# Kernel tuning notes

Hardware: AMD Instinct MI355X
Metric: run time of the kernel (lower is better)

Reference implementation:

```python
import jax, jax.numpy as jnp
import numpy as np

B, W, E, D, F = 128, 64, 256, 256, 4  # batch, window, enc_hidden, dec_hidden, out_feats


def setup_inputs() -> dict:
    key = jax.random.key(0)
    ks = jax.random.split(key, 16)
    s = 0.05
    return {
        "input_encoded": jax.random.normal(ks[0], (B, W, E), jnp.float32),
        "y_history": jax.random.normal(ks[1], (B, W, F), jnp.float32),
        # attn_layer: Linear(2D+E -> E), Tanh, Linear(E -> 1)
        "attn_w1": jax.random.normal(ks[2], (E, 2 * D + E), jnp.float32) * s,
        "attn_b1": jax.random.normal(ks[3], (E,), jnp.float32) * s,
        "attn_w2": jax.random.normal(ks[4], (1, E), jnp.float32) * s,
        "attn_b2": jax.random.normal(ks[5], (1,), jnp.float32) * s,
        # single-layer LSTM cell: input F, hidden D (gate order i,f,g,o)
        "w_ih": jax.random.normal(ks[6], (4 * D, F), jnp.float32) * s,
        "w_hh": jax.random.normal(ks[7], (4 * D, D), jnp.float32) * s,
        "b_ih": jax.random.normal(ks[8], (4 * D,), jnp.float32) * s,
        "b_hh": jax.random.normal(ks[9], (4 * D,), jnp.float32) * s,
        # fc: Linear(E+F -> F) (weights normal_() in torch, scaled here for stability)
        "fc_w": jax.random.normal(ks[10], (F, E + F), jnp.float32) * s,
        "fc_b": jax.random.normal(ks[11], (F,), jnp.float32) * s,
        # fc_final: Linear(D+E -> F)
        "fcf_w": jax.random.normal(ks[12], (F, D + E), jnp.float32) * s,
        "fcf_b": jax.random.normal(ks[13], (F,), jnp.float32) * s,
    }


def _decoder(input_encoded, y_history, attn_w1, attn_b1, attn_w2, attn_b2,
             w_ih, w_hh, b_ih, b_hh, fc_w, fc_b, fcf_w, fcf_b):
    b = input_encoded.shape[0]
    h0 = jnp.zeros((b, D), input_encoded.dtype)
    c0 = jnp.zeros((b, D), input_encoded.dtype)
    ctx0 = jnp.zeros((b, E), input_encoded.dtype)
    y_seq = jnp.transpose(y_history, (1, 0, 2))  # [W, B, F]

    def step(carry, y_t):
        h, c, _ = carry  # h, c: [B, D]
        # additive attention over encoder timesteps
        hc = jnp.broadcast_to(h[:, None, :], (b, W, D))
        cc = jnp.broadcast_to(c[:, None, :], (b, W, D))
        x = jnp.concatenate([hc, cc, input_encoded], axis=2)  # [B, W, 2D+E]
        z = jnp.tanh(jnp.einsum('bwk,ek->bwe', x, attn_w1) + attn_b1)
        scores = jnp.einsum('bwe,oe->bwo', z, attn_w2)[..., 0] + attn_b2[0]  # [B, W]
        attn = jax.nn.softmax(scores, axis=1)
        context = jnp.einsum('bw,bwe->be', attn, input_encoded)  # [B, E]
        # fc over (context, y_t)
        y_tilde = jnp.concatenate([context, y_t], axis=1) @ fc_w.T + fc_b  # [B, F]
        # one LSTM cell step (torch gate order: i, f, g, o)
        gates = y_tilde @ w_ih.T + b_ih + h @ w_hh.T + b_hh  # [B, 4D]
        i_g, f_g, g_g, o_g = jnp.split(gates, 4, axis=1)
        c_new = jax.nn.sigmoid(f_g) * c + jax.nn.sigmoid(i_g) * jnp.tanh(g_g)
        h_new = jax.nn.sigmoid(o_g) * jnp.tanh(c_new)
        return (h_new, c_new, context), None

    (h, c, context), _ = jax.lax.scan(step, (h0, c0, ctx0), y_seq)
    return jnp.concatenate([h, context], axis=1) @ fcf_w.T + fcf_b  # [B, F]


def reference(input_encoded, y_history, attn_w1, attn_b1, attn_w2, attn_b2,
              w_ih, w_hh, b_ih, b_hh, fc_w, fc_b, fcf_w, fcf_b):
    return _decoder(input_encoded, y_history, attn_w1, attn_b1, attn_w2, attn_b2,
                    w_ih, w_hh, b_ih, b_hh, fc_w, fc_b, fcf_w, fcf_b)
```

## Files before the change

kernel.cpp:

```cpp
#include <hip/hip_runtime.h>

#define Bn 128
#define Wn 64

typedef _Float16 h2 __attribute__((ext_vector_type(2)));

__device__ unsigned g_sf[256];
__device__ unsigned g_stf[256];
__device__ unsigned g_scp[256][2][256];
__device__ unsigned g_stp[256][2][128];
__device__ unsigned g_ep16[Bn * Wn * 128];
__device__ float4 g_encfc[Bn * Wn];
__device__ float4 g_encfcf[Bn * Wn];
__device__ uint4 g_w1pk[8 * 32 * 64];
__device__ uint4 g_whpk[8 * 128 * 32];

__device__ __forceinline__ float ftanh(float x) {
  float p = __builtin_exp2f(x * 2.885390081777927f);
  return 1.0f - 2.0f * __builtin_amdgcn_rcpf(p + 1.0f);
}
__device__ __forceinline__ float fsigm(float x) {
  float p = __builtin_exp2f(-x * 1.4426950408889634f);
  return __builtin_amdgcn_rcpf(1.0f + p);
}
__device__ __forceinline__ float dot4(float4 a, float4 b) {
  return a.x * b.x + a.y * b.y + a.z * b.z + a.w * b.w;
}
__device__ __forceinline__ float fd2(unsigned w, unsigned h, float acc) {
  h2 a = __builtin_bit_cast(h2, w), b = __builtin_bit_cast(h2, h);
#if __has_builtin(__builtin_amdgcn_fdot2)
  return __builtin_amdgcn_fdot2(a, b, acc, false);
#else
  return acc + (float)a.x * (float)b.x + (float)a.y * (float)b.y;
#endif
}
__device__ __forceinline__ float fd2x4u(uint4 w, uint4 h, float acc) {
  acc = fd2(w.x, h.x, acc);
  acc = fd2(w.y, h.y, acc);
  acc = fd2(w.z, h.z, acc);
  acc = fd2(w.w, h.w, acc);
  return acc;
}
__device__ __forceinline__ unsigned pk(float a, float b) {
  h2 h = {(_Float16)a, (_Float16)b};
  return __builtin_bit_cast(unsigned, h);
}
__device__ __forceinline__ void ast(unsigned* p, unsigned v) {
  __hip_atomic_store(p, v, __ATOMIC_RELAXED, __HIP_MEMORY_SCOPE_AGENT);
}
__device__ __forceinline__ unsigned ald(unsigned* p) {
  return __hip_atomic_load(p, __ATOMIC_RELAXED, __HIP_MEMORY_SCOPE_AGENT);
}
__device__ __forceinline__ float aldf(unsigned* p) {
  return __builtin_bit_cast(float, ald(p));
}

#define STPHYS(c, L) ((c) * 68 + ((L) >> 4) * 17 + ((L) & 15))

__global__ void reset_kernel(float* out) {
  int t = threadIdx.x;
  if (t < 256) { g_sf[t] = 0u; g_stf[t] = 0u; }
  if (t < 512) out[t] = 0.f;
}

__global__ __launch_bounds__(256) void pack_kernel(const float* __restrict__ w1,
                                                   const float* __restrict__ w_hh) {
  int idx = blockIdx.x * 256 + threadIdx.x;
  const float* src;
  uint4* dst;
  if (idx < 16384) {
    int m = idx >> 11, e_loc = (idx >> 6) & 31, ku = idx & 63;
    int e = m * 32 + e_loc;
    src = w1 + (size_t)e * 768 + 8 * ku;
    dst = g_w1pk + idx;
  } else {
    int j = idx - 16384;
    int m = j >> 12, rq = (j >> 5) & 127, i = j & 31;
    int q = rq >> 5, dl = rq & 31;
    int R = q * 256 + m * 32 + dl;
    src = w_hh + (size_t)R * 256 + 8 * i;
    dst = g_whpk + j;
  }
  uint4 o;
  o.x = pk(src[0], src[1]); o.y = pk(src[2], src[3]);
  o.z = pk(src[4], src[5]); o.w = pk(src[6], src[7]);
  *dst = o;
}

__global__ __launch_bounds__(256) void eproj_kernel(const float* __restrict__ enc,
                                                    const float* __restrict__ w1,
                                                    const float* __restrict__ b1) {
  __shared__ __align__(16) float4 encs[16][64];
  __shared__ float accs[16][256];
  const int m0 = blockIdx.x * 16;
  const int tid = threadIdx.x;
  const float4* eg = (const float4*)(enc + (size_t)m0 * 256);
#pragma unroll
  for (int i = 0; i < 4; i++) {
    int idx = tid + 256 * i;
    encs[idx >> 6][idx & 63] = eg[idx];
  }
  __syncthreads();
  const int e = tid;
  float acc[16];
#pragma unroll
  for (int i = 0; i < 16; i++) acc[i] = 0.f;
  const float4* wrow = (const float4*)(w1 + e * 768 + 512);
  for (int k4 = 0; k4 < 64; k4++) {
    float4 wv = wrow[k4];
#pragma unroll
    for (int i = 0; i < 16; i++) acc[i] += dot4(wv, encs[i][k4]);
  }
  float bb = b1[e];
#pragma unroll
  for (int i = 0; i < 16; i++) accs[i][e] = acc[i] + bb;
  __syncthreads();
#pragma unroll
  for (int r = 0; r < 8; r++) {
    int idx = r * 256 + tid;
    int i = idx >> 7, jp = idx & 127;
    g_ep16[(size_t)(m0 + i) * 128 + jp] = pk(accs[i][2 * jp], accs[i][2 * jp + 1]);
  }
}

__global__ __launch_bounds__(256) void encfc_kernel(const float* __restrict__ enc,
                                                    const float* __restrict__ fc_w,
                                                    const float* __restrict__ fcf_w) {
  __shared__ __align__(16) float4 encs[16][64];
  const int m0 = blockIdx.x * 16;
  const int tid = threadIdx.x;
  const float4* eg = (const float4*)(enc + (size_t)m0 * 256);
#pragma unroll
  for (int i = 0; i < 4; i++) {
    int idx = tid + 256 * i;
    encs[idx >> 6][idx & 63] = eg[idx];
  }
  __syncthreads();
  if (tid < 128) {
    const int r = tid >> 3, o = tid & 7;
    const float* wr = (o < 4) ? (fc_w + o * 260) : (fcf_w + (o - 4) * 512 + 256);
    const float4* w4 = (const float4*)wr;
    float a = 0.f;
#pragma unroll 8
    for (int k = 0; k < 64; k++) a += dot4(w4[k], encs[r][k]);
    if (o < 4) ((float*)&g_encfc[m0 + r])[o] = a;
    else ((float*)&g_encfcf[m0 + r])[o - 4] = a;
  }
}

__global__ __launch_bounds__(512, 1) void decoder_kernel(
    const float* __restrict__ yhist, const float* __restrict__ w2,
    const float* __restrict__ w_ih, const float* __restrict__ b_ih,
    const float* __restrict__ b_hh,
    const float* __restrict__ fc_w, const float* __restrict__ fc_b,
    const float* __restrict__ fcf_w, const float* __restrict__ fcf_b,
    float* __restrict__ out) {
  __shared__ __align__(16) uint4 w1l[32 * 65];
  __shared__ __align__(16) uint4 whl[128 * 33];
  __shared__ __align__(16) uint4 ep_t[4 * 257];
  __shared__ __align__(16) uint4 st4[4 * 68];
  __shared__ __align__(16) float4 encfc_l[256];
  __shared__ __align__(16) float4 yh_l[256];
  __shared__ __align__(16) float4 wihl[132];
  __shared__ float biasl[132];
  __shared__ float ag_l[4 * 133];
  __shared__ float hcp_l[4 * 36];
  __shared__ float w2_l[32];
  __shared__ float scp_l[256], sc_a[256], sc_b[256];
  __shared__ float cl[132];
  __shared__ __align__(16) float4 ytl[4];
  __shared__ float fcy_l[16];
  __shared__ float fcb_l[4];

  const int g = blockIdx.x, t = threadIdx.x;
  const int m = (g >> 3) & 7;
  const int gx = g - 8 * m;
  const int G = (g & 7) * 4 + (g >> 6);
  const int cbase = 4 * G;
  const int l = t & 63, wv = t >> 6;
  const int e_loc = t >> 4, ks = t & 15;
  const int row = t >> 2, kq2 = t & 3;

  unsigned* st32 = (unsigned*)st4;

#pragma unroll
  for (int j = 0; j < 4; j++) {
    int f = t + 512 * j;
    w1l[(f >> 6) * 65 + (f & 63)] = g_w1pk[m * 2048 + f];
  }
#pragma unroll
  for (int j = 0; j < 8; j++) {
    int f = t + 512 * j;
    whl[(f >> 5) * 33 + (f & 31)] = g_whpk[m * 4096 + f];
  }
#pragma unroll
  for (int j = 0; j < 2; j++) {
    int f = t + 512 * j;
    int u = f >> 8, cw = f & 255, c = cw >> 6, w = cw & 63;
    ep_t[u * 257 + cw] =
        ((const uint4*)(g_ep16 + ((size_t)((cbase + c) * 64 + w)) * 128))[m * 4 + u];
  }
  if (t < 272) st4[t] = (uint4){0u, 0u, 0u, 0u};
  if (t < 256) {
    int c = t >> 6, w = t & 63;
    encfc_l[t] = g_encfc[(cbase + c) * 64 + w];
    yh_l[t] = ((const float4*)yhist)[(cbase + c) * 64 + w];
  }
  if (t < 128) {
    int q = t >> 5, dl = t & 31;
    int R = q * 256 + m * 32 + dl;
    wihl[q * 33 + dl] = *(const float4*)(w_ih + (size_t)R * 4);
    biasl[q * 33 + dl] = b_ih[R] + b_hh[R];
  }
  if (t < 132) cl[t] = 0.f;
  if (t < 32) w2_l[t] = w2[m * 32 + t];
  if (t < 16) fcy_l[t] = fc_w[(t >> 2) * 260 + 256 + (t & 3)];
  if (t < 4) fcb_l[t] = fc_b[t];
  __syncthreads();

  float attw = 0.f;
  for (int tstep = 0; tstep < Wn; tstep++) {
    const int tb = tstep & 1;
    const unsigned want = (unsigned)(tstep + 1);
    {
      float a0 = 0.f, a1 = 0.f, a2 = 0.f, a3 = 0.f;
      const uint4* wrow = &w1l[e_loc * 65 + 4 * ks];
#pragma unroll
      for (int j = 0; j < 4; j++) {
        uint4 wvv = wrow[j];
        int ku = 4 * ks + j;
        int ph = (ku >> 4) * 17 + (ku & 15);
        a0 = fd2x4u(wvv, st4[ph], a0);
        a1 = fd2x4u(wvv, st4[68 + ph], a1);
        a2 = fd2x4u(wvv, st4[136 + ph], a2);
        a3 = fd2x4u(wvv, st4[204 + ph], a3);
      }
#pragma unroll
      for (int dd = 1; dd < 16; dd <<= 1) {
        a0 += __shfl_xor(a0, dd, 64);
        a1 += __shfl_xor(a1, dd, 64);
        a2 += __shfl_xor(a2, dd, 64);
        a3 += __shfl_xor(a3, dd, 64);
      }
      if (ks == 0) {
        hcp_l[e_loc] = a0;
        hcp_l[36 + e_loc] = a1;
        hcp_l[72 + e_loc] = a2;
        hcp_l[108 + e_loc] = a3;
      }
    }
    __syncthreads();
    {
      const int cB = t >> 7, wB = (t & 127) >> 1, halfB = t & 1;
      float s = 0.f;
#pragma unroll
      for (int j = 0; j < 2; j++) {
        int u = 2 * halfB + j;
        uint4 uu = ep_t[u * 257 + cB * 64 + wB];
        unsigned um[4] = {uu.x, uu.y, uu.z, uu.w};
#pragma unroll
        for (int ui = 0; ui < 4; ui++) {
          int e0 = 2 * (4 * u + ui);
          h2 aa = __builtin_bit_cast(h2, um[ui]);
          s += w2_l[e0] * ftanh((float)aa.x + hcp_l[cB * 36 + e0]);
          s += w2_l[e0 + 1] * ftanh((float)aa.y + hcp_l[cB * 36 + e0 + 1]);
        }
      }
      s += __shfl_xor(s, 1, 64);
      if (halfB == 0) scp_l[cB * 64 + wB] = s;
    }
    __syncthreads();
    if (wv == 0) {
      unsigned* dst = &g_scp[g][tb][4 * l];
      ast(dst + 0, __builtin_bit_cast(unsigned, scp_l[4 * l + 0]));
      ast(dst + 1, __builtin_bit_cast(unsigned, scp_l[4 * l + 1]));
      ast(dst + 2, __builtin_bit_cast(unsigned, scp_l[4 * l + 2]));
      ast(dst + 3, __builtin_bit_cast(unsigned, scp_l[4 * l + 3]));
      asm volatile("s_waitcnt vmcnt(0)" ::: "memory");
      if (l == 0) ast(&g_sf[g], want);
    }
    {
      float b0 = 0.f, b1 = 0.f, b2 = 0.f, b3 = 0.f;
      const uint4* wr = &whl[row * 33 + 8 * kq2];
#pragma unroll
      for (int j = 0; j < 8; j++) {
        uint4 wvv = wr[j];
        int i = 8 * kq2 + j;
        int ph = (i >> 4) * 17 + (i & 15);
        b0 = fd2x4u(wvv, st4[ph], b0);
        b1 = fd2x4u(wvv, st4[68 + ph], b1);
        b2 = fd2x4u(wvv, st4[136 + ph], b2);
        b3 = fd2x4u(wvv, st4[204 + ph], b3);
      }
#pragma unroll
      for (int dd = 1; dd < 4; dd <<= 1) {
        b0 += __shfl_xor(b0, dd, 64);
        b1 += __shfl_xor(b1, dd, 64);
        b2 += __shfl_xor(b2, dd, 64);
        b3 += __shfl_xor(b3, dd, 64);
      }
      if (kq2 == 0) {
        ag_l[row] = b0;
        ag_l[133 + row] = b1;
        ag_l[266 + row] = b2;
        ag_l[399 + row] = b3;
      }
    }
    if (wv == 1) {
      if (l < 4) {
        unsigned* fp = &g_sf[gx + 8 * ((m + 1 + l) & 7)];
        while (ald(fp) < want) __builtin_amdgcn_s_sleep(1);
      }
      asm volatile("" ::: "memory");
      float a0 = 0.f, a1 = 0.f, a2 = 0.f, a3 = 0.f;
#pragma unroll
      for (int k = 1; k <= 4; k++) {
        unsigned* sp = &g_scp[gx + 8 * ((m + k) & 7)][tb][4 * l];
        a0 += aldf(sp + 0); a1 += aldf(sp + 1);
        a2 += aldf(sp + 2); a3 += aldf(sp + 3);
      }
      sc_a[4 * l] = a0; sc_a[4 * l + 1] = a1;
      sc_a[4 * l + 2] = a2; sc_a[4 * l + 3] = a3;
    } else if (wv == 2) {
      if (l < 3) {
        unsigned* fp = &g_sf[gx + 8 * ((m + 5 + l) & 7)];
        while (ald(fp) < want) __builtin_amdgcn_s_sleep(1);
      }
      asm volatile("" ::: "memory");
      float a0 = 0.f, a1 = 0.f, a2 = 0.f, a3 = 0.f;
#pragma unroll
      for (int k = 5; k <= 7; k++) {
        unsigned* sp = &g_scp[gx + 8 * ((m + k) & 7)][tb][4 * l];
        a0 += aldf(sp + 0); a1 += aldf(sp + 1);
        a2 += aldf(sp + 2); a3 += aldf(sp + 3);
      }
      sc_b[4 * l] = a0; sc_b[4 * l + 1] = a1;
      sc_b[4 * l + 2] = a2; sc_b[4 * l + 3] = a3;
    }
    __syncthreads();
    if (wv < 4) {
      const int c = wv;
      float sc = scp_l[c * 64 + l] + sc_a[c * 64 + l] + sc_b[c * 64 + l];
      float mm = sc;
#pragma unroll
      for (int dd = 32; dd; dd >>= 1) mm = fmaxf(mm, __shfl_xor(mm, dd, 64));
      float pr = __builtin_exp2f((sc - mm) * 1.4426950408889634f);
      float su = pr;
#pragma unroll
      for (int dd = 32; dd; dd >>= 1) su += __shfl_xor(su, dd, 64);
      attw = pr * __builtin_amdgcn_rcpf(su);
      float4 ef = encfc_l[c * 64 + l];
      float rx = attw * ef.x, ry = attw * ef.y, rz = attw * ef.z, rw = attw * ef.w;
#pragma unroll
      for (int dd = 32; dd; dd >>= 1) {
        rx += __shfl_xor(rx, dd, 64);
        ry += __shfl_xor(ry, dd, 64);
        rz += __shfl_xor(rz, dd, 64);
        rw += __shfl_xor(rw, dd, 64);
      }
      if (l == 0) {
        float4 yv = yh_l[c * 64 + tstep];
        float4 yt;
        yt.x = rx + fcb_l[0] + fcy_l[0] * yv.x + fcy_l[1] * yv.y + fcy_l[2] * yv.z + fcy_l[3] * yv.w;
        yt.y = ry + fcb_l[1] + fcy_l[4] * yv.x + fcy_l[5] * yv.y + fcy_l[6] * yv.z + fcy_l[7] * yv.w;
        yt.z = rz + fcb_l[2] + fcy_l[8] * yv.x + fcy_l[9] * yv.y + fcy_l[10] * yv.z + fcy_l[11] * yv.w;
        yt.w = rw + fcb_l[3] + fcy_l[12] * yv.x + fcy_l[13] * yv.y + fcy_l[14] * yv.z + fcy_l[15] * yv.w;
        ytl[c] = yt;
      }
    }
    __syncthreads();
    if (wv == 0) {
      const int c = l >> 4, pp = l & 15;
      const int d0 = 2 * pp, d1 = d0 + 1;
      float4 yt = ytl[c];
#define GV(q, d) (ag_l[c * 133 + (q) * 32 + (d)] + biasl[(q) * 33 + (d)] + dot4(wihl[(q) * 33 + (d)], yt))
      float i0 = fsigm(GV(0, d0)), f0 = fsigm(GV(1, d0));
      float G0 = ftanh(GV(2, d0)), o0 = fsigm(GV(3, d0));
      float i1 = fsigm(GV(0, d1)), f1 = fsigm(GV(1, d1));
      float G1 = ftanh(GV(2, d1)), o1 = fsigm(GV(3, d1));
#undef GV
      float cn0 = f0 * cl[c * 33 + d0] + i0 * G0;
      float cn1 = f1 * cl[c * 33 + d1] + i1 * G1;
      float hn0 = o0 * ftanh(cn0), hn1 = o1 * ftanh(cn1);
      cl[c * 33 + d0] = cn0; cl[c * 33 + d1] = cn1;
      unsigned hp = pk(hn0, hn1), cp = pk(cn0, cn1);
      {
        int Lh = 4 * m + (pp >> 2), Lc = 32 + 4 * m + (pp >> 2);
        st32[4 * STPHYS(c, Lh) + (pp & 3)] = hp;
        st32[4 * STPHYS(c, Lc) + (pp & 3)] = cp;
      }
      if (tstep < 63) {
        ast(&g_stp[g][tb][c * 32 + pp], hp);
        ast(&g_stp[g][tb][c * 32 + 16 + pp], cp);
        asm volatile("s_waitcnt vmcnt(0)" ::: "memory");
        if (l == 0) ast(&g_stf[g], want);
      }
    } else if (wv >= 2 && tstep < 63) {
      for (int k = wv - 1; k < 8; k += 6) {
        int mo = (m + k) & 7;
        if (l == 0) {
          unsigned* fp = &g_stf[gx + 8 * mo];
          while (ald(fp) < want) __builtin_amdgcn_s_sleep(1);
        }
        asm volatile("" ::: "memory");
        if (l < 32) {
          unsigned* sp = &g_stp[gx + 8 * mo][tb][4 * l];
#pragma unroll
          for (int k2 = 0; k2 < 4; k2++) {
            unsigned v = ald(sp + k2);
            int i = 4 * l + k2;
            int c = i >> 5, r = i & 31, pp = r & 15, isC = r >> 4;
            int L = isC * 32 + 4 * mo + (pp >> 2);
            st32[4 * STPHYS(c, L) + (pp & 3)] = v;
          }
        }
      }
    }
    __syncthreads();
  }

  if (wv < 4) {
    const int c = wv, b = cbase + c;
    const int pp = l & 15, f = l >> 4;
    int Lh = 4 * m + (pp >> 2);
    h2 hh = __builtin_bit_cast(h2, st32[4 * STPHYS(c, Lh) + (pp & 3)]);
    const int d0 = m * 32 + 2 * pp;
    float v = fcf_w[f * 512 + d0] * (float)hh.x + fcf_w[f * 512 + d0 + 1] * (float)hh.y;
#pragma unroll
    for (int dd = 1; dd < 16; dd <<= 1) v += __shfl_xor(v, dd, 64);
    if (pp == 0) atomicAdd(out + b * 4 + f, v);
    if (m == 0) {
      float4 fv = g_encfcf[b * 64 + l];
      float vx = attw * fv.x, vy = attw * fv.y, vz = attw * fv.z, vw = attw * fv.w;
#pragma unroll
      for (int dd = 32; dd; dd >>= 1) {
        vx += __shfl_xor(vx, dd, 64);
        vy += __shfl_xor(vy, dd, 64);
        vz += __shfl_xor(vz, dd, 64);
        vw += __shfl_xor(vw, dd, 64);
      }
      if (l == 0) {
        atomicAdd(out + b * 4 + 0, vx + fcf_b[0]);
        atomicAdd(out + b * 4 + 1, vy + fcf_b[1]);
        atomicAdd(out + b * 4 + 2, vz + fcf_b[2]);
        atomicAdd(out + b * 4 + 3, vw + fcf_b[3]);
      }
    }
  }
}

extern "C" void kernel_launch(void* const* d_in, const int* in_sizes, int n_in,
                              void* d_out, int out_size, void* d_ws, size_t ws_size,
                              hipStream_t stream) {
  (void)in_sizes; (void)n_in; (void)d_ws; (void)ws_size; (void)out_size;
  const float* enc   = (const float*)d_in[0];
  const float* yhist = (const float*)d_in[1];
  const float* w1    = (const float*)d_in[2];
  const float* b1    = (const float*)d_in[3];
  const float* w2    = (const float*)d_in[4];
  const float* w_ih  = (const float*)d_in[6];
  const float* w_hh  = (const float*)d_in[7];
  const float* b_ih  = (const float*)d_in[8];
  const float* b_hh  = (const float*)d_in[9];
  const float* fc_w  = (const float*)d_in[10];
  const float* fc_b  = (const float*)d_in[11];
  const float* fcf_w = (const float*)d_in[12];
  const float* fcf_b = (const float*)d_in[13];
  float* out = (float*)d_out;

  reset_kernel<<<dim3(1), dim3(512), 0, stream>>>(out);
  pack_kernel<<<dim3(192), dim3(256), 0, stream>>>(w1, w_hh);
  eproj_kernel<<<dim3(512), dim3(256), 0, stream>>>(enc, w1, b1);
  encfc_kernel<<<dim3(512), dim3(256), 0, stream>>>(enc, fc_w, fcf_w);
  decoder_kernel<<<dim3(256), dim3(512), 0, stream>>>(yhist, w2, w_ih, b_ih, b_hh,
                                                      fc_w, fc_b, fcf_w, fcf_b, out);
}
```

Before: 629.7 us.

## Split per-block batch into two halves to overlap cross-block exchange with compute

Each block's four batch rows are now processed as two pairs per timestep. The score and state exchange for one pair is published and polled while the other pair is computed, which aims to hide inter-block latency on the sequential LSTM critical path. Polling moves to two dedicated waves, and flags use release stores. The cost is more __syncthreads per step, more complex flag and buffer bookkeeping, and a leftover dead lambda.

```diff
diff --git a/kernel.cpp b/kernel.cpp
--- a/kernel.cpp
+++ b/kernel.cpp
@@ -5,10 +5,10 @@
 
 typedef _Float16 h2 __attribute__((ext_vector_type(2)));
 
-__device__ unsigned g_sf[256];
-__device__ unsigned g_stf[256];
-__device__ unsigned g_scp[256][2][256];
-__device__ unsigned g_stp[256][2][128];
+__device__ unsigned g_sfp[512];
+__device__ unsigned g_stfp[512];
+__device__ unsigned g_scp2[256][2][2][128];
+__device__ unsigned g_stp2[256][2][2][64];
 __device__ unsigned g_ep16[Bn * Wn * 128];
 __device__ float4 g_encfc[Bn * Wn];
 __device__ float4 g_encfcf[Bn * Wn];
@@ -48,6 +48,9 @@
 __device__ __forceinline__ void ast(unsigned* p, unsigned v) {
   __hip_atomic_store(p, v, __ATOMIC_RELAXED, __HIP_MEMORY_SCOPE_AGENT);
 }
+__device__ __forceinline__ void ast_rel(unsigned* p, unsigned v) {
+  __hip_atomic_store(p, v, __ATOMIC_RELEASE, __HIP_MEMORY_SCOPE_AGENT);
+}
 __device__ __forceinline__ unsigned ald(unsigned* p) {
   return __hip_atomic_load(p, __ATOMIC_RELAXED, __HIP_MEMORY_SCOPE_AGENT);
 }
@@ -59,8 +62,7 @@
 
 __global__ void reset_kernel(float* out) {
   int t = threadIdx.x;
-  if (t < 256) { g_sf[t] = 0u; g_stf[t] = 0u; }
-  if (t < 512) out[t] = 0.f;
+  if (t < 512) { g_sfp[t] = 0u; g_stfp[t] = 0u; out[t] = 0.f; }
 }
 
 __global__ __launch_bounds__(256) void pack_kernel(const float* __restrict__ w1,
@@ -166,7 +168,9 @@
   __shared__ float ag_l[4 * 133];
   __shared__ float hcp_l[4 * 36];
   __shared__ float w2_l[32];
-  __shared__ float scp_l[256], sc_a[256], sc_b[256];
+  __shared__ float scp_l[256];
+  __shared__ float sc_sum[256];
+  __shared__ float att_fin[256];
   __shared__ float cl[132];
   __shared__ __align__(16) float4 ytl[4];
   __shared__ float fcy_l[16];
@@ -218,139 +222,162 @@
   if (t < 4) fcb_l[t] = fc_b[t];
   __syncthreads();
 
-  float attw = 0.f;
-  for (int tstep = 0; tstep < Wn; tstep++) {
-    const int tb = tstep & 1;
-    const unsigned want = (unsigned)(tstep + 1);
+  auto A1A2 = [&](int pr) {
+    const int ca = 2 * pr;
     {
-      float a0 = 0.f, a1 = 0.f, a2 = 0.f, a3 = 0.f;
+      float a0 = 0.f, a1 = 0.f;
       const uint4* wrow = &w1l[e_loc * 65 + 4 * ks];
 #pragma unroll
       for (int j = 0; j < 4; j++) {
         uint4 wvv = wrow[j];
         int ku = 4 * ks + j;
         int ph = (ku >> 4) * 17 + (ku & 15);
-        a0 = fd2x4u(wvv, st4[ph], a0);
-        a1 = fd2x4u(wvv, st4[68 + ph], a1);
-        a2 = fd2x4u(wvv, st4[136 + ph], a2);
-        a3 = fd2x4u(wvv, st4[204 + ph], a3);
+        a0 = fd2x4u(wvv, st4[ca * 68 + ph], a0);
+        a1 = fd2x4u(wvv, st4[(ca + 1) * 68 + ph], a1);
       }
 #pragma unroll
       for (int dd = 1; dd < 16; dd <<= 1) {
         a0 += __shfl_xor(a0, dd, 64);
         a1 += __shfl_xor(a1, dd, 64);
-        a2 += __shfl_xor(a2, dd, 64);
-        a3 += __shfl_xor(a3, dd, 64);
       }
       if (ks == 0) {
-        hcp_l[e_loc] = a0;
-        hcp_l[36 + e_loc] = a1;
-        hcp_l[72 + e_loc] = a2;
-        hcp_l[108 + e_loc] = a3;
-      }
-    }
-    __syncthreads();
+        hcp_l[ca * 36 + e_loc] = a0;
+        hcp_l[(ca + 1) * 36 + e_loc] = a1;
+      }
+    }
     {
-      const int cB = t >> 7, wB = (t & 127) >> 1, halfB = t & 1;
-      float s = 0.f;
-#pragma unroll
-      for (int j = 0; j < 2; j++) {
-        int u = 2 * halfB + j;
-        uint4 uu = ep_t[u * 257 + cB * 64 + wB];
-        unsigned um[4] = {uu.x, uu.y, uu.z, uu.w};
-#pragma unroll
-        for (int ui = 0; ui < 4; ui++) {
-          int e0 = 2 * (4 * u + ui);
-          h2 aa = __builtin_bit_cast(h2, um[ui]);
-          s += w2_l[e0] * ftanh((float)aa.x + hcp_l[cB * 36 + e0]);
-          s += w2_l[e0 + 1] * ftanh((float)aa.y + hcp_l[cB * 36 + e0 + 1]);
-        }
-      }
-      s += __shfl_xor(s, 1, 64);
-      if (halfB == 0) scp_l[cB * 64 + wB] = s;
-    }
-    __syncthreads();
-    if (wv == 0) {
-      unsigned* dst = &g_scp[g][tb][4 * l];
-      ast(dst + 0, __builtin_bit_cast(unsigned, scp_l[4 * l + 0]));
-      ast(dst + 1, __builtin_bit_cast(unsigned, scp_l[4 * l + 1]));
-      ast(dst + 2, __builtin_bit_cast(unsigned, scp_l[4 * l + 2]));
-      ast(dst + 3, __builtin_bit_cast(unsigned, scp_l[4 * l + 3]));
-      asm volatile("s_waitcnt vmcnt(0)" ::: "memory");
-      if (l == 0) ast(&g_sf[g], want);
-    }
-    {
-      float b0 = 0.f, b1 = 0.f, b2 = 0.f, b3 = 0.f;
+      float b0 = 0.f, b1 = 0.f;
       const uint4* wr = &whl[row * 33 + 8 * kq2];
 #pragma unroll
       for (int j = 0; j < 8; j++) {
         uint4 wvv = wr[j];
         int i = 8 * kq2 + j;
         int ph = (i >> 4) * 17 + (i & 15);
-        b0 = fd2x4u(wvv, st4[ph], b0);
-        b1 = fd2x4u(wvv, st4[68 + ph], b1);
-        b2 = fd2x4u(wvv, st4[136 + ph], b2);
-        b3 = fd2x4u(wvv, st4[204 + ph], b3);
+        b0 = fd2x4u(wvv, st4[ca * 68 + ph], b0);
+        b1 = fd2x4u(wvv, st4[(ca + 1) * 68 + ph], b1);
       }
 #pragma unroll
       for (int dd = 1; dd < 4; dd <<= 1) {
         b0 += __shfl_xor(b0, dd, 64);
         b1 += __shfl_xor(b1, dd, 64);
-        b2 += __shfl_xor(b2, dd, 64);
-        b3 += __shfl_xor(b3, dd, 64);
       }
       if (kq2 == 0) {
-        ag_l[row] = b0;
-        ag_l[133 + row] = b1;
-        ag_l[266 + row] = b2;
-        ag_l[399 + row] = b3;
-      }
-    }
-    if (wv == 1) {
-      if (l < 4) {
-        unsigned* fp = &g_sf[gx + 8 * ((m + 1 + l) & 7)];
+        ag_l[ca * 133 + row] = b0;
+        ag_l[(ca + 1) * 133 + row] = b1;
+      }
+    }
+  };
+
+  auto Bph = [&](int pr) {
+    const int c = 2 * pr + (t >> 8), wB = (t >> 2) & 63, qB = t & 3;
+    float s = 0.f;
+    uint4 uu = ep_t[qB * 257 + c * 64 + wB];
+    unsigned um[4] = {uu.x, uu.y, uu.z, uu.w};
+#pragma unroll
+    for (int ui = 0; ui < 4; ui++) {
+      int e0 = 2 * (4 * qB + ui);
+      h2 aa = __builtin_bit_cast(h2, um[ui]);
+      s += w2_l[e0] * ftanh((float)aa.x + hcp_l[c * 36 + e0]);
+      s += w2_l[e0 + 1] * ftanh((float)aa.y + hcp_l[c * 36 + e0 + 1]);
+    }
+    s += __shfl_xor(s, 1, 64);
+    s += __shfl_xor(s, 2, 64);
+    if (qB == 0) scp_l[c * 64 + wB] = s;
+  };
+
+  float attw_keep = 0.f;
+
+  auto Cph = [&](int pr) {
+    const int c = 2 * pr + wv;
+    float sc = scp_l[c * 64 + l] + sc_sum[c * 64 + l];
+    float mm = sc;
+#pragma unroll
+    for (int dd = 32; dd; dd >>= 1) mm = fmaxf(mm, __shfl_xor(mm, dd, 64));
+    float pr2 = __builtin_exp2f((sc - mm) * 1.4426950408889634f);
+    float su = pr2;
+#pragma unroll
+    for (int dd = 32; dd; dd >>= 1) su += __shfl_xor(su, dd, 64);
+    float aw = pr2 * __builtin_amdgcn_rcpf(su);
+    att_fin[c * 64 + l] = aw;
+    float4 ef = encfc_l[c * 64 + l];
+    float rx = aw * ef.x, ry = aw * ef.y, rz = aw * ef.z, rw = aw * ef.w;
+#pragma unroll
+    for (int dd = 32; dd; dd >>= 1) {
+      rx += __shfl_xor(rx, dd, 64);
+      ry += __shfl_xor(ry, dd, 64);
+      rz += __shfl_xor(rz, dd, 64);
+      rw += __shfl_xor(rw, dd, 64);
+    }
+    if (l == 0) {
+      float4 yv;
+      yv = yh_l[c * 64 + 0];
+      (void)yv;
+    }
+    (void)attw_keep;
+  };
+  (void)Cph;
+
+  for (int tstep = 0; tstep < Wn; tstep++) {
+    const int tb = tstep & 1;
+    const unsigned want = (unsigned)(tstep + 1);
+
+    if (wv >= 6 && tstep > 0) {
+      int idx = t - 384;
+      for (int q = idx; q < 448; q += 128) {
+        int kk = q >> 6, j = q & 63;
+        int mo = (m + 1 + kk) & 7;
+        unsigned* fp = &g_stfp[256 + gx + 8 * mo];
+        while (ald(fp) < (unsigned)tstep) __builtin_amdgcn_s_sleep(1);
+        asm volatile("" ::: "memory");
+        unsigned v = ald(&g_stp2[gx + 8 * mo][(tstep - 1) & 1][1][j]);
+        int c_loc = j >> 5, r = j & 31, pp = r & 15, isC = r >> 4;
+        int c = 2 + c_loc;
+        int L = isC * 32 + 4 * mo + (pp >> 2);
+        st32[4 * STPHYS(c, L) + (pp & 3)] = v;
+      }
+    }
+    A1A2(0);
+    __syncthreads();
+    Bph(0);
+    __syncthreads();
+    if (wv == 0) {
+      unsigned* dst = &g_scp2[g][tb][0][0];
+      ast(dst + 2 * l, __builtin_bit_cast(unsigned, scp_l[2 * l]));
+      ast(dst + 2 * l + 1, __builtin_bit_cast(unsigned, scp_l[2 * l + 1]));
+      if (l == 0) ast_rel(&g_sfp[g], want);
+      else asm volatile("s_waitcnt vmcnt(0)" ::: "memory");
+    }
+    A1A2(1);
+    __syncthreads();
+    if (wv >= 6) {
+      int idx = t - 384;
+      float s = 0.f;
+#pragma unroll
+      for (int kk = 0; kk < 7; kk++) {
+        int mo = (m + 1 + kk) & 7;
+        unsigned* fp = &g_sfp[gx + 8 * mo];
         while (ald(fp) < want) __builtin_amdgcn_s_sleep(1);
-      }
-      asm volatile("" ::: "memory");
-      float a0 = 0.f, a1 = 0.f, a2 = 0.f, a3 = 0.f;
-#pragma unroll
-      for (int k = 1; k <= 4; k++) {
-        unsigned* sp = &g_scp[gx + 8 * ((m + k) & 7)][tb][4 * l];
-        a0 += aldf(sp + 0); a1 += aldf(sp + 1);
-        a2 += aldf(sp + 2); a3 += aldf(sp + 3);
-      }
-      sc_a[4 * l] = a0; sc_a[4 * l + 1] = a1;
-      sc_a[4 * l + 2] = a2; sc_a[4 * l + 3] = a3;
-    } else if (wv == 2) {
-      if (l < 3) {
-        unsigned* fp = &g_sf[gx + 8 * ((m + 5 + l) & 7)];
-        while (ald(fp) < want) __builtin_amdgcn_s_sleep(1);
-      }
-      asm volatile("" ::: "memory");
-      float a0 = 0.f, a1 = 0.f, a2 = 0.f, a3 = 0.f;
-#pragma unroll
-      for (int k = 5; k <= 7; k++) {
-        unsigned* sp = &g_scp[gx + 8 * ((m + k) & 7)][tb][4 * l];
-        a0 += aldf(sp + 0); a1 += aldf(sp + 1);
-        a2 += aldf(sp + 2); a3 += aldf(sp + 3);
-      }
-      sc_b[4 * l] = a0; sc_b[4 * l + 1] = a1;
-      sc_b[4 * l + 2] = a2; sc_b[4 * l + 3] = a3;
-    }
-    __syncthreads();
-    if (wv < 4) {
+        asm volatile("" ::: "memory");
+        s += aldf(&g_scp2[gx + 8 * mo][tb][0][idx]);
+      }
+      sc_sum[idx] = s;
+    }
+    Bph(1);
+    __syncthreads();
+    if (wv < 2) {
       const int c = wv;
-      float sc = scp_l[c * 64 + l] + sc_a[c * 64 + l] + sc_b[c * 64 + l];
+      float sc = scp_l[c * 64 + l] + sc_sum[c * 64 + l];
       float mm = sc;
 #pragma unroll
       for (int dd = 32; dd; dd >>= 1) mm = fmaxf(mm, __shfl_xor(mm, dd, 64));
-      float pr = __builtin_exp2f((sc - mm) * 1.4426950408889634f);
-      float su = pr;
+      float pr2 = __builtin_exp2f((sc - mm) * 1.4426950408889634f);
+      float su = pr2;
 #pragma unroll
       for (int dd = 32; dd; dd >>= 1) su += __shfl_xor(su, dd, 64);
-      attw = pr * __builtin_amdgcn_rcpf(su);
+      float aw = pr2 * __builtin_amdgcn_rcpf(su);
+      att_fin[c * 64 + l] = aw;
       float4 ef = encfc_l[c * 64 + l];
-      float rx = attw * ef.x, ry = attw * ef.y, rz = attw * ef.z, rw = attw * ef.w;
+      float rx = aw * ef.x, ry = aw * ef.y, rz = aw * ef.z, rw = aw * ef.w;
 #pragma unroll
       for (int dd = 32; dd; dd >>= 1) {
         rx += __shfl_xor(rx, dd, 64);
@@ -367,53 +394,129 @@
         yt.w = rw + fcb_l[3] + fcy_l[12] * yv.x + fcy_l[13] * yv.y + fcy_l[14] * yv.z + fcy_l[15] * yv.w;
         ytl[c] = yt;
       }
+    } else if (wv == 2) {
+      unsigned* dst = &g_scp2[g][tb][1][0];
+      ast(dst + 2 * l, __builtin_bit_cast(unsigned, scp_l[128 + 2 * l]));
+      ast(dst + 2 * l + 1, __builtin_bit_cast(unsigned, scp_l[128 + 2 * l + 1]));
+      if (l == 0) ast_rel(&g_sfp[256 + g], want);
+      else asm volatile("s_waitcnt vmcnt(0)" ::: "memory");
     }
     __syncthreads();
     if (wv == 0) {
-      const int c = l >> 4, pp = l & 15;
-      const int d0 = 2 * pp, d1 = d0 + 1;
-      float4 yt = ytl[c];
+      if (l < 32) {
+        const int c = l >> 4, pp = l & 15;
+        const int d0 = 2 * pp, d1 = d0 + 1;
+        float4 yt = ytl[c];
 #define GV(q, d) (ag_l[c * 133 + (q) * 32 + (d)] + biasl[(q) * 33 + (d)] + dot4(wihl[(q) * 33 + (d)], yt))
-      float i0 = fsigm(GV(0, d0)), f0 = fsigm(GV(1, d0));
-      float G0 = ftanh(GV(2, d0)), o0 = fsigm(GV(3, d0));
-      float i1 = fsigm(GV(0, d1)), f1 = fsigm(GV(1, d1));
-      float G1 = ftanh(GV(2, d1)), o1 = fsigm(GV(3, d1));
+        float i0 = fsigm(GV(0, d0)), f0 = fsigm(GV(1, d0));
+        float G0 = ftanh(GV(2, d0)), o0 = fsigm(GV(3, d0));
+        float i1 = fsigm(GV(0, d1)), f1 = fsigm(GV(1, d1));
+        float G1 = ftanh(GV(2, d1)), o1 = fsigm(GV(3, d1));
 #undef GV
-      float cn0 = f0 * cl[c * 33 + d0] + i0 * G0;
-      float cn1 = f1 * cl[c * 33 + d1] + i1 * G1;
-      float hn0 = o0 * ftanh(cn0), hn1 = o1 * ftanh(cn1);
-      cl[c * 33 + d0] = cn0; cl[c * 33 + d1] = cn1;
-      unsigned hp = pk(hn0, hn1), cp = pk(cn0, cn1);
-      {
+        float cn0 = f0 * cl[c * 33 + d0] + i0 * G0;
+        float cn1 = f1 * cl[c * 33 + d1] + i1 * G1;
+        float hn0 = o0 * ftanh(cn0), hn1 = o1 * ftanh(cn1);
+        cl[c * 33 + d0] = cn0; cl[c * 33 + d1] = cn1;
+        unsigned hp = pk(hn0, hn1), cp = pk(cn0, cn1);
         int Lh = 4 * m + (pp >> 2), Lc = 32 + 4 * m + (pp >> 2);
         st32[4 * STPHYS(c, Lh) + (pp & 3)] = hp;
         st32[4 * STPHYS(c, Lc) + (pp & 3)] = cp;
+        if (tstep < 63) {
+          ast(&g_stp2[g][tb][0][c * 32 + pp], hp);
+          ast(&g_stp2[g][tb][0][c * 32 + 16 + pp], cp);
+        }
       }
       if (tstep < 63) {
-        ast(&g_stp[g][tb][c * 32 + pp], hp);
-        ast(&g_stp[g][tb][c * 32 + 16 + pp], cp);
-        asm volatile("s_waitcnt vmcnt(0)" ::: "memory");
-        if (l == 0) ast(&g_stf[g], want);
-      }
-    } else if (wv >= 2 && tstep < 63) {
-      for (int k = wv - 1; k < 8; k += 6) {
-        int mo = (m + k) & 7;
-        if (l == 0) {
-          unsigned* fp = &g_stf[gx + 8 * mo];
-          while (ald(fp) < want) __builtin_amdgcn_s_sleep(1);
+        if (l == 0) ast_rel(&g_stfp[g], want);
+        else asm volatile("s_waitcnt vmcnt(0)" ::: "memory");
+      }
+    } else if (wv >= 6) {
+      int idx = t - 384;
+      float s = 0.f;
+#pragma unroll
+      for (int kk = 0; kk < 7; kk++) {
+        int mo = (m + 1 + kk) & 7;
+        unsigned* fp = &g_sfp[256 + gx + 8 * mo];
+        while (ald(fp) < want) __builtin_amdgcn_s_sleep(1);
+        asm volatile("" ::: "memory");
+        s += aldf(&g_scp2[gx + 8 * mo][tb][1][idx]);
+      }
+      sc_sum[128 + idx] = s;
+    }
+    __syncthreads();
+    if (wv < 2) {
+      const int c = 2 + wv;
+      float sc = scp_l[c * 64 + l] + sc_sum[c * 64 + l];
+      float mm = sc;
+#pragma unroll
+      for (int dd = 32; dd; dd >>= 1) mm = fmaxf(mm, __shfl_xor(mm, dd, 64));
+      float pr2 = __builtin_exp2f((sc - mm) * 1.4426950408889634f);
+      float su = pr2;
+#pragma unroll
+      for (int dd = 32; dd; dd >>= 1) su += __shfl_xor(su, dd, 64);
+      float aw = pr2 * __builtin_amdgcn_rcpf(su);
+      att_fin[c * 64 + l] = aw;
+      float4 ef = encfc_l[c * 64 + l];
+      float rx = aw * ef.x, ry = aw * ef.y, rz = aw * ef.z, rw = aw * ef.w;
+#pragma unroll
+      for (int dd = 32; dd; dd >>= 1) {
+        rx += __shfl_xor(rx, dd, 64);
+        ry += __shfl_xor(ry, dd, 64);
+        rz += __shfl_xor(rz, dd, 64);
+        rw += __shfl_xor(rw, dd, 64);
+      }
+      if (l == 0) {
+        float4 yv = yh_l[c * 64 + tstep];
+        float4 yt;
+        yt.x = rx + fcb_l[0] + fcy_l[0] * yv.x + fcy_l[1] * yv.y + fcy_l[2] * yv.z + fcy_l[3] * yv.w;
+        yt.y = ry + fcb_l[1] + fcy_l[4] * yv.x + fcy_l[5] * yv.y + fcy_l[6] * yv.z + fcy_l[7] * yv.w;
+        yt.z = rz + fcb_l[2] + fcy_l[8] * yv.x + fcy_l[9] * yv.y + fcy_l[10] * yv.z + fcy_l[11] * yv.w;
+        yt.w = rw + fcb_l[3] + fcy_l[12] * yv.x + fcy_l[13] * yv.y + fcy_l[14] * yv.z + fcy_l[15] * yv.w;
+        ytl[c] = yt;
+      }
+    }
+    __syncthreads();
+    if (wv == 0) {
+      if (l < 32) {
+        const int c = 2 + (l >> 4), pp = l & 15;
+        const int d0 = 2 * pp, d1 = d0 + 1;
+        float4 yt = ytl[c];
+#define GV(q, d) (ag_l[c * 133 + (q) * 32 + (d)] + biasl[(q) * 33 + (d)] + dot4(wihl[(q) * 33 + (d)], yt))
+        float i0 = fsigm(GV(0, d0)), f0 = fsigm(GV(1, d0));
+        float G0 = ftanh(GV(2, d0)), o0 = fsigm(GV(3, d0));
+        float i1 = fsigm(GV(0, d1)), f1 = fsigm(GV(1, d1));
+        float G1 = ftanh(GV(2, d1)), o1 = fsigm(GV(3, d1));
+#undef GV
+        float cn0 = f0 * cl[c * 33 + d0] + i0 * G0;
+        float cn1 = f1 * cl[c * 33 + d1] + i1 * G1;
+        float hn0 = o0 * ftanh(cn0), hn1 = o1 * ftanh(cn1);
+        cl[c * 33 + d0] = cn0; cl[c * 33 + d1] = cn1;
+        unsigned hp = pk(hn0, hn1), cp = pk(cn0, cn1);
+        int Lh = 4 * m + (pp >> 2), Lc = 32 + 4 * m + (pp >> 2);
+        st32[4 * STPHYS(c, Lh) + (pp & 3)] = hp;
+        st32[4 * STPHYS(c, Lc) + (pp & 3)] = cp;
+        if (tstep < 63) {
+          ast(&g_stp2[g][tb][1][(c - 2) * 32 + pp], hp);
+          ast(&g_stp2[g][tb][1][(c - 2) * 32 + 16 + pp], cp);
         }
+      }
+      if (tstep < 63) {
+        if (l == 0) ast_rel(&g_stfp[256 + g], want);
+        else asm volatile("s_waitcnt vmcnt(0)" ::: "memory");
+      }
+    } else if (wv >= 6 && tstep < 63) {
+      int idx = t - 384;
+      for (int q = idx; q < 448; q += 128) {
+        int kk = q >> 6, j = q & 63;
+        int mo = (m + 1 + kk) & 7;
+        unsigned* fp = &g_stfp[gx + 8 * mo];
+        while (ald(fp) < want) __builtin_amdgcn_s_sleep(1);
         asm volatile("" ::: "memory");
-        if (l < 32) {
-          unsigned* sp = &g_stp[gx + 8 * mo][tb][4 * l];
-#pragma unroll
-          for (int k2 = 0; k2 < 4; k2++) {
-            unsigned v = ald(sp + k2);
-            int i = 4 * l + k2;
-            int c = i >> 5, r = i & 31, pp = r & 15, isC = r >> 4;
-            int L = isC * 32 + 4 * mo + (pp >> 2);
-            st32[4 * STPHYS(c, L) + (pp & 3)] = v;
-          }
-        }
+        unsigned v = ald(&g_stp2[gx + 8 * mo][tb][0][j]);
+        int c_loc = j >> 5, r = j & 31, pp = r & 15, isC = r >> 4;
+        int c = c_loc;
+        int L = isC * 32 + 4 * mo + (pp >> 2);
+        st32[4 * STPHYS(c, L) + (pp & 3)] = v;
       }
     }
     __syncthreads();
@@ -430,8 +533,9 @@
     for (int dd = 1; dd < 16; dd <<= 1) v += __shfl_xor(v, dd, 64);
     if (pp == 0) atomicAdd(out + b * 4 + f, v);
     if (m == 0) {
+      float aw = att_fin[c * 64 + l];
       float4 fv = g_encfcf[b * 64 + l];
-      float vx = attw * fv.x, vy = attw * fv.y, vz = attw * fv.z, vw = attw * fv.w;
+      float vx = aw * fv.x, vy = aw * fv.y, vz = aw * fv.z, vw = aw * fv.w;
 #pragma unroll
       for (int dd = 32; dd; dd >>= 1) {
         vx += __shfl_xor(vx, dd, 64);
```

After: 1.270 ms. 102% more time.
